# Performance work log

Hardware: AMD Instinct MI355X
Metric: run time of the kernel (lower is better)

Reference implementation:

```python
import jax, jax.numpy as jnp
import numpy as np
import math

B, I, O, D, H = 32, 1152, 10, 16, 10
SUB = 0.8
S = math.ceil(SUB * I)  # 922 subset size


def _safe_l2norm(x, axis, keepdims=False):
    # L2 norm with zero-safe gradient (forward-identical to jnp.linalg.norm)
    s = jnp.sum(x * x, axis=axis, keepdims=keepdims)
    return jnp.where(s == 0, 0.0, jnp.sqrt(jnp.where(s == 0, 1.0, s)))


def setup_inputs() -> dict:
    key = jax.random.key(0)
    k1, k2 = jax.random.split(key)
    u_predict = jax.random.normal(k1, (B, I, O, D), dtype=jnp.float32)
    # emulate torch.rand(...).topk(S, dim=1).indices: top-S distinct indices along input_caps
    noise = jax.random.uniform(k2, (B, I, O, H))
    sample_idx = jnp.argsort(-noise, axis=1)[:, :S].astype(jnp.int64)  # [B,S,O,H]
    return {"u_predict": u_predict, "sample_idx": sample_idx}


def reference(u_predict, sample_idx):
    b, i, o, d = u_predict.shape
    h = sample_idx.shape[-1]
    # scatter 0/1 hypothesis mask r: [B,I,O,H]
    bi = jnp.arange(b)[:, None, None, None]
    oi = jnp.arange(o)[None, None, :, None]
    hi = jnp.arange(h)[None, None, None, :]
    r = jnp.zeros((b, i, o, h), u_predict.dtype).at[bi, sample_idx, oi, hi].set(1.0)

    # Vr = V_exp * r; since r is 0/1, ||Vr||_D = r * ||V||_D
    Vnorm = _safe_l2norm(u_predict, axis=3)            # [B,I,O]
    Vr_norm = Vnorm[..., None] * r                     # [B,I,O,H]
    # Mu = sum_i(Vr_norm * Vr) / sum_i Vr_norm  (Vr_norm*Vr = r*||V||*V since r^2=r)
    num = jnp.einsum('bioh,biod->bodh', Vr_norm, u_predict)   # [B,O,D,H]
    Mu = num / jnp.sum(Vr_norm, axis=1)[:, :, None, :]        # [B,O,D,H]

    # losses = sum_i ||V_exp - Mu||_D  -> [B,O,H]
    diff = u_predict[..., None] - Mu[:, None]          # [B,I,O,D,H]
    losses = jnp.sum(_safe_l2norm(diff, axis=3), axis=1)
    min_idx = jnp.argmin(losses, axis=2)               # [B,O]

    # pick best hypothesis's mask per (batch, output_caps)
    final_r = jnp.take_along_axis(r, min_idx[:, None, :, None], axis=3)  # [B,I,O,1]

    # capsule weighted average
    u = u_predict * final_r
    un = _safe_l2norm(u, axis=3, keepdims=True)        # [B,I,O,1]
    v = jnp.sum(u * un, axis=1) / jnp.sum(un, axis=1)  # [B,O,D]
    return v
```

## Files before the change

### kernel.cpp

```cpp
#include <hip/hip_runtime.h>
#include <math.h>


#define B_    32
#define I_    1152
#define O_    10
#define D_    16
#define H_    10
#define S_    922
#define MASKW 36
#define NT    640

__global__ __launch_bounds__(NT, 1) void ransac_kernel(
    const float* __restrict__ up,
    const int*   __restrict__ sidx,
    float*       __restrict__ out)
{
    __shared__ float    u_t[D_][I_];
    __shared__ float    vn[I_];
    __shared__ unsigned mask[H_][MASKW];
    __shared__ float    Mu[D_][H_];
    __shared__ double   losses[H_];
    __shared__ int      hstar;

    const int bo   = blockIdx.x;
    const int b    = bo / O_;
    const int o    = bo - b * O_;
    const int tid  = threadIdx.x;
    const int lane = tid & 63;
    const int wv   = tid >> 6;

    for (int j = tid; j < H_ * MASKW; j += NT)
        ((unsigned*)mask)[j] = 0u;
    __syncthreads();

    const int* sb = sidx + (size_t)b * (S_ * O_ * H_) + o * H_;
    for (int j = tid; j < S_ * H_; j += NT) {
        int s = j / H_;
        int h = j - s * H_;
        int idx = sb[s * (O_ * H_) + h];
        atomicOr(&mask[h][idx >> 5], 1u << (idx & 31));
    }

    const float* ub = up + (size_t)b * (I_ * O_ * D_) + o * D_;
    for (int i = tid; i < I_; i += NT) {
        const float4* p = (const float4*)(ub + (size_t)i * (O_ * D_));
        float4 q0 = p[0], q1 = p[1], q2 = p[2], q3 = p[3];
        float s = q0.x*q0.x + q0.y*q0.y + q0.z*q0.z + q0.w*q0.w
                + q1.x*q1.x + q1.y*q1.y + q1.z*q1.z + q1.w*q1.w
                + q2.x*q2.x + q2.y*q2.y + q2.z*q2.z + q2.w*q2.w
                + q3.x*q3.x + q3.y*q3.y + q3.z*q3.z + q3.w*q3.w;
        vn[i] = sqrtf(s);
        u_t[ 0][i]=q0.x; u_t[ 1][i]=q0.y; u_t[ 2][i]=q0.z; u_t[ 3][i]=q0.w;
        u_t[ 4][i]=q1.x; u_t[ 5][i]=q1.y; u_t[ 6][i]=q1.z; u_t[ 7][i]=q1.w;
        u_t[ 8][i]=q2.x; u_t[ 9][i]=q2.y; u_t[10][i]=q2.z; u_t[11][i]=q2.w;
        u_t[12][i]=q3.x; u_t[13][i]=q3.y; u_t[14][i]=q3.z; u_t[15][i]=q3.w;
    }
    __syncthreads();

    const int h = wv;
    float num[D_];
    #pragma unroll
    for (int d = 0; d < D_; ++d) num[d] = 0.f;
    float den = 0.f;
    for (int i = lane; i < I_; i += 64) {
        unsigned bit = (mask[h][i >> 5] >> (i & 31)) & 1u;
        float w = bit ? vn[i] : 0.f;
        den += w;
        #pragma unroll
        for (int d = 0; d < D_; ++d) num[d] = fmaf(w, u_t[d][i], num[d]);
    }
    #pragma unroll
    for (int off = 32; off; off >>= 1) {
        den += __shfl_xor(den, off, 64);
        #pragma unroll
        for (int d = 0; d < D_; ++d) num[d] += __shfl_xor(num[d], off, 64);
    }
    if (lane == 0) {
        float rd = 1.f / den;
        #pragma unroll
        for (int d = 0; d < D_; ++d) Mu[d][h] = num[d] * rd;
    }
    __syncthreads();

    float muh[D_];
    #pragma unroll
    for (int d = 0; d < D_; ++d) muh[d] = Mu[d][h];
    double loss = 0.0;
    for (int i = lane; i < I_; i += 64) {
        float ss = 0.f;
        #pragma unroll
        for (int d = 0; d < D_; ++d) {
            float df = u_t[d][i] - muh[d];
            ss = fmaf(df, df, ss);
        }
        loss += sqrt((double)ss);
    }
    #pragma unroll
    for (int off = 32; off; off >>= 1)
        loss += __shfl_xor(loss, off, 64);
    if (lane == 0) losses[h] = loss;
    __syncthreads();

    if (tid == 0) {
        int best = 0; double bl = losses[0];
        #pragma unroll
        for (int hh = 1; hh < H_; ++hh)
            if (losses[hh] < bl) { bl = losses[hh]; best = hh; }
        hstar = best;
    }
    __syncthreads();

    if (tid < D_)
        out[(size_t)bo * D_ + tid] = Mu[tid][hstar];
}

extern "C" void kernel_launch(void* const* d_in, const int* in_sizes, int n_in,
                              void* d_out, int out_size, void* d_ws, size_t ws_size,
                              hipStream_t stream) {
    const float* up   = (const float*)d_in[0];
    const int*   sidx = (const int*)d_in[1];
    float*       out  = (float*)d_out;
    ransac_kernel<<<B_ * O_, NT, 0, stream>>>(up, sidx, out);
}
```

Before: 113.0 us.

## Compute hypothesis means via complement lists and expand loss distances algebraically

```diff
diff --git a/kernel.cpp b/kernel.cpp
--- a/kernel.cpp
+++ b/kernel.cpp
@@ -8,41 +8,82 @@
 #define D_    16
 #define H_    10
 #define S_    922
+#define COMP  230
 #define MASKW 36
-#define NT    640
-
-__global__ __launch_bounds__(NT, 1) void ransac_kernel(
+#define NT    512
+#define NW    8
+
+__device__ __forceinline__ int uoff(int i, int c) {
+    return i * 16 + (((c ^ ((i >> 1) & 3)) & 3) << 2);
+}
+
+template <int CTRL, int ROWM>
+static __device__ __forceinline__ float dpp_f(float v) {
+    return __int_as_float(__builtin_amdgcn_update_dpp(
+        0, __float_as_int(v), CTRL, ROWM, 0xf, true));
+}
+static __device__ __forceinline__ float wave_sum_f32(float v) {
+    v += dpp_f<0x111, 0xf>(v);
+    v += dpp_f<0x112, 0xf>(v);
+    v += dpp_f<0x114, 0xf>(v);
+    v += dpp_f<0x118, 0xf>(v);
+    v += dpp_f<0x142, 0xa>(v);
+    v += dpp_f<0x143, 0xc>(v);
+    return v;
+}
+template <int CTRL, int ROWM>
+static __device__ __forceinline__ double dpp_d(double v) {
+    long long x = __double_as_longlong(v);
+    int lo = (int)(unsigned)(x & 0xffffffffLL);
+    int hi = (int)(x >> 32);
+    lo = __builtin_amdgcn_update_dpp(0, lo, CTRL, ROWM, 0xf, true);
+    hi = __builtin_amdgcn_update_dpp(0, hi, CTRL, ROWM, 0xf, true);
+    return __longlong_as_double((long long)(unsigned)lo | ((long long)hi << 32));
+}
+static __device__ __forceinline__ double wave_sum_f64(double v) {
+    v += dpp_d<0x111, 0xf>(v);
+    v += dpp_d<0x112, 0xf>(v);
+    v += dpp_d<0x114, 0xf>(v);
+    v += dpp_d<0x118, 0xf>(v);
+    v += dpp_d<0x142, 0xa>(v);
+    v += dpp_d<0x143, 0xc>(v);
+    return v;
+}
+
+__global__ __launch_bounds__(NT, 2) void ransac_kernel(
     const float* __restrict__ up,
     const int*   __restrict__ sidx,
     float*       __restrict__ out)
 {
-    __shared__ float    u_t[D_][I_];
-    __shared__ float    vn[I_];
-    __shared__ unsigned mask[H_][MASKW];
-    __shared__ float    Mu[D_][H_];
-    __shared__ double   losses[H_];
-    __shared__ int      hstar;
-
-    const int bo   = blockIdx.x;
-    const int b    = bo / O_;
-    const int o    = bo - b * O_;
+    __shared__ float          u_s[I_ * 16];
+    __shared__ unsigned       mask[H_][MASKW];
+    __shared__ unsigned short clist[H_][COMP];
+    __shared__ int            ccount[H_];
+    __shared__ float          Mu_s[H_][D_];
+    __shared__ float          totred[NW][17];
+    __shared__ float          tot[17];
+    __shared__ double         lpart[H_][NW];
+    __shared__ double         losses[H_];
+    __shared__ int            hstar;
+
+    const int blk = blockIdx.x;
+    const int xcd = blk & 7, g = blk >> 3;
+    const int b   = xcd + 8 * (g / O_);
+    const int o   = g - O_ * (g / O_);
+    const int bo  = b * O_ + o;
+
     const int tid  = threadIdx.x;
     const int lane = tid & 63;
     const int wv   = tid >> 6;
 
-    for (int j = tid; j < H_ * MASKW; j += NT)
-        ((unsigned*)mask)[j] = 0u;
-    __syncthreads();
-
-    const int* sb = sidx + (size_t)b * (S_ * O_ * H_) + o * H_;
-    for (int j = tid; j < S_ * H_; j += NT) {
-        int s = j / H_;
-        int h = j - s * H_;
-        int idx = sb[s * (O_ * H_) + h];
-        atomicOr(&mask[h][idx >> 5], 1u << (idx & 31));
-    }
-
-    const float* ub = up + (size_t)b * (I_ * O_ * D_) + o * D_;
+    for (int j = tid; j < H_ * MASKW; j += NT) ((unsigned*)mask)[j] = 0u;
+    if (tid < H_) ccount[tid] = 0;
+    __syncthreads();
+
+    const float* ub = up + ((size_t)b * I_ * O_ + o) * D_;
+    float acc[D_]; float accd = 0.f;
+    #pragma unroll
+    for (int d = 0; d < D_; ++d) acc[d] = 0.f;
     for (int i = tid; i < I_; i += NT) {
         const float4* p = (const float4*)(ub + (size_t)i * (O_ * D_));
         float4 q0 = p[0], q1 = p[1], q2 = p[2], q3 = p[3];
@@ -50,69 +91,170 @@
                 + q1.x*q1.x + q1.y*q1.y + q1.z*q1.z + q1.w*q1.w
                 + q2.x*q2.x + q2.y*q2.y + q2.z*q2.z + q2.w*q2.w
                 + q3.x*q3.x + q3.y*q3.y + q3.z*q3.z + q3.w*q3.w;
-        vn[i] = sqrtf(s);
-        u_t[ 0][i]=q0.x; u_t[ 1][i]=q0.y; u_t[ 2][i]=q0.z; u_t[ 3][i]=q0.w;
-        u_t[ 4][i]=q1.x; u_t[ 5][i]=q1.y; u_t[ 6][i]=q1.z; u_t[ 7][i]=q1.w;
-        u_t[ 8][i]=q2.x; u_t[ 9][i]=q2.y; u_t[10][i]=q2.z; u_t[11][i]=q2.w;
-        u_t[12][i]=q3.x; u_t[13][i]=q3.y; u_t[14][i]=q3.z; u_t[15][i]=q3.w;
-    }
-    __syncthreads();
-
-    const int h = wv;
-    float num[D_];
-    #pragma unroll
-    for (int d = 0; d < D_; ++d) num[d] = 0.f;
-    float den = 0.f;
-    for (int i = lane; i < I_; i += 64) {
-        unsigned bit = (mask[h][i >> 5] >> (i & 31)) & 1u;
-        float w = bit ? vn[i] : 0.f;
-        den += w;
-        #pragma unroll
-        for (int d = 0; d < D_; ++d) num[d] = fmaf(w, u_t[d][i], num[d]);
-    }
-    #pragma unroll
-    for (int off = 32; off; off >>= 1) {
-        den += __shfl_xor(den, off, 64);
-        #pragma unroll
-        for (int d = 0; d < D_; ++d) num[d] += __shfl_xor(num[d], off, 64);
-    }
-    if (lane == 0) {
-        float rd = 1.f / den;
-        #pragma unroll
-        for (int d = 0; d < D_; ++d) Mu[d][h] = num[d] * rd;
-    }
-    __syncthreads();
-
-    float muh[D_];
-    #pragma unroll
-    for (int d = 0; d < D_; ++d) muh[d] = Mu[d][h];
-    double loss = 0.0;
-    for (int i = lane; i < I_; i += 64) {
-        float ss = 0.f;
-        #pragma unroll
-        for (int d = 0; d < D_; ++d) {
-            float df = u_t[d][i] - muh[d];
-            ss = fmaf(df, df, ss);
-        }
-        loss += sqrt((double)ss);
-    }
-    #pragma unroll
-    for (int off = 32; off; off >>= 1)
-        loss += __shfl_xor(loss, off, 64);
-    if (lane == 0) losses[h] = loss;
-    __syncthreads();
-
+        float vn = sqrtf(s);
+        *(float4*)&u_s[uoff(i,0)] = q0;
+        *(float4*)&u_s[uoff(i,1)] = q1;
+        *(float4*)&u_s[uoff(i,2)] = q2;
+        *(float4*)&u_s[uoff(i,3)] = q3;
+        acc[ 0] = fmaf(vn, q0.x, acc[ 0]); acc[ 1] = fmaf(vn, q0.y, acc[ 1]);
+        acc[ 2] = fmaf(vn, q0.z, acc[ 2]); acc[ 3] = fmaf(vn, q0.w, acc[ 3]);
+        acc[ 4] = fmaf(vn, q1.x, acc[ 4]); acc[ 5] = fmaf(vn, q1.y, acc[ 5]);
+        acc[ 6] = fmaf(vn, q1.z, acc[ 6]); acc[ 7] = fmaf(vn, q1.w, acc[ 7]);
+        acc[ 8] = fmaf(vn, q2.x, acc[ 8]); acc[ 9] = fmaf(vn, q2.y, acc[ 9]);
+        acc[10] = fmaf(vn, q2.z, acc[10]); acc[11] = fmaf(vn, q2.w, acc[11]);
+        acc[12] = fmaf(vn, q3.x, acc[12]); acc[13] = fmaf(vn, q3.y, acc[13]);
+        acc[14] = fmaf(vn, q3.z, acc[14]); acc[15] = fmaf(vn, q3.w, acc[15]);
+        accd += vn;
+    }
+
+    const int* sb = sidx + (size_t)b * (S_ * O_ * H_) + o * H_;
+    for (int j = tid; j < S_ * H_; j += NT) {
+        int s = j / H_;
+        int h = j - s * H_;
+        int idx = sb[s * (O_ * H_) + h];
+        atomicOr(&mask[h][idx >> 5], 1u << (idx & 31));
+    }
+
+    #pragma unroll
+    for (int d = 0; d < D_; ++d) acc[d] = wave_sum_f32(acc[d]);
+    accd = wave_sum_f32(accd);
+    if (lane == 63) {
+        #pragma unroll
+        for (int d = 0; d < D_; ++d) totred[wv][d] = acc[d];
+        totred[wv][16] = accd;
+    }
+    __syncthreads();
+
+    if (tid < 17) {
+        float t = 0.f;
+        #pragma unroll
+        for (int w = 0; w < NW; ++w) t += totred[w][tid];
+        tot[tid] = t;
+    }
+
+    for (int h = wv; h < H_; h += NW) {
+        if (lane < MASKW) {
+            unsigned m = ~mask[h][lane];
+            int cnt = __popc(m);
+            int base = atomicAdd(&ccount[h], cnt);
+            while (m) {
+                int bit = __ffs(m) - 1;
+                m &= m - 1u;
+                clist[h][base++] = (unsigned short)((lane << 5) + bit);
+            }
+        }
+    }
+    __syncthreads();
+
+    for (int h = wv; h < H_; h += NW) {
+        float na[D_]; float nd = 0.f;
+        #pragma unroll
+        for (int d = 0; d < D_; ++d) na[d] = 0.f;
+        for (int k = lane; k < COMP; k += 64) {
+            int i = clist[h][k];
+            float4 q0 = *(const float4*)&u_s[uoff(i,0)];
+            float4 q1 = *(const float4*)&u_s[uoff(i,1)];
+            float4 q2 = *(const float4*)&u_s[uoff(i,2)];
+            float4 q3 = *(const float4*)&u_s[uoff(i,3)];
+            float s = q0.x*q0.x + q0.y*q0.y + q0.z*q0.z + q0.w*q0.w
+                    + q1.x*q1.x + q1.y*q1.y + q1.z*q1.z + q1.w*q1.w
+                    + q2.x*q2.x + q2.y*q2.y + q2.z*q2.z + q2.w*q2.w
+                    + q3.x*q3.x + q3.y*q3.y + q3.z*q3.z + q3.w*q3.w;
+            float vn = sqrtf(s);
+            na[ 0] = fmaf(vn, q0.x, na[ 0]); na[ 1] = fmaf(vn, q0.y, na[ 1]);
+            na[ 2] = fmaf(vn, q0.z, na[ 2]); na[ 3] = fmaf(vn, q0.w, na[ 3]);
+            na[ 4] = fmaf(vn, q1.x, na[ 4]); na[ 5] = fmaf(vn, q1.y, na[ 5]);
+            na[ 6] = fmaf(vn, q1.z, na[ 6]); na[ 7] = fmaf(vn, q1.w, na[ 7]);
+            na[ 8] = fmaf(vn, q2.x, na[ 8]); na[ 9] = fmaf(vn, q2.y, na[ 9]);
+            na[10] = fmaf(vn, q2.z, na[10]); na[11] = fmaf(vn, q2.w, na[11]);
+            na[12] = fmaf(vn, q3.x, na[12]); na[13] = fmaf(vn, q3.y, na[13]);
+            na[14] = fmaf(vn, q3.z, na[14]); na[15] = fmaf(vn, q3.w, na[15]);
+            nd += vn;
+        }
+        #pragma unroll
+        for (int d = 0; d < D_; ++d) na[d] = wave_sum_f32(na[d]);
+        nd = wave_sum_f32(nd);
+        if (lane == 63) {
+            float rd = 1.f / (tot[16] - nd);
+            #pragma unroll
+            for (int d = 0; d < D_; ++d)
+                Mu_s[h][d] = (tot[d] - na[d]) * rd;
+        }
+    }
+    __syncthreads();
+
+    float mu[H_][D_];
+    #pragma unroll
+    for (int h = 0; h < H_; ++h) {
+        float4 m0 = *(const float4*)&Mu_s[h][0];
+        float4 m1 = *(const float4*)&Mu_s[h][4];
+        float4 m2 = *(const float4*)&Mu_s[h][8];
+        float4 m3 = *(const float4*)&Mu_s[h][12];
+        mu[h][ 0]=m0.x; mu[h][ 1]=m0.y; mu[h][ 2]=m0.z; mu[h][ 3]=m0.w;
+        mu[h][ 4]=m1.x; mu[h][ 5]=m1.y; mu[h][ 6]=m1.z; mu[h][ 7]=m1.w;
+        mu[h][ 8]=m2.x; mu[h][ 9]=m2.y; mu[h][10]=m2.z; mu[h][11]=m2.w;
+        mu[h][12]=m3.x; mu[h][13]=m3.y; mu[h][14]=m3.z; mu[h][15]=m3.w;
+    }
+    float musq[H_];
+    #pragma unroll
+    for (int h = 0; h < H_; ++h) {
+        float s = 0.f;
+        #pragma unroll
+        for (int d = 0; d < D_; ++d) s = fmaf(mu[h][d], mu[h][d], s);
+        musq[h] = s;
+    }
+    double lacc[H_];
+    #pragma unroll
+    for (int h = 0; h < H_; ++h) lacc[h] = 0.0;
+
+    auto lossStep = [&](int i) {
+        float4 q0 = *(const float4*)&u_s[uoff(i,0)];
+        float4 q1 = *(const float4*)&u_s[uoff(i,1)];
+        float4 q2 = *(const float4*)&u_s[uoff(i,2)];
+        float4 q3 = *(const float4*)&u_s[uoff(i,3)];
+        float uq[D_] = {q0.x,q0.y,q0.z,q0.w, q1.x,q1.y,q1.z,q1.w,
+                        q2.x,q2.y,q2.z,q2.w, q3.x,q3.y,q3.z,q3.w};
+        float usq = 0.f;
+        #pragma unroll
+        for (int d = 0; d < D_; ++d) usq = fmaf(uq[d], uq[d], usq);
+        #pragma unroll
+        for (int h = 0; h < H_; ++h) {
+            float dot = 0.f;
+            #pragma unroll
+            for (int d = 0; d < D_; ++d) dot = fmaf(uq[d], mu[h][d], dot);
+            float d2 = fmaf(-2.f, dot, usq + musq[h]);
+            lacc[h] += (double)sqrtf(fmaxf(d2, 0.f));
+        }
+    };
+    lossStep(tid);
+    lossStep(tid + NT);
+    if (tid >= 384) lossStep(tid + 640);
+
+    #pragma unroll
+    for (int h = 0; h < H_; ++h) lacc[h] = wave_sum_f64(lacc[h]);
+    if (lane == 63) {
+        #pragma unroll
+        for (int h = 0; h < H_; ++h) lpart[h][wv] = lacc[h];
+    }
+    __syncthreads();
+
+    if (tid < H_) {
+        double t = 0.0;
+        #pragma unroll
+        for (int w = 0; w < NW; ++w) t += lpart[tid][w];
+        losses[tid] = t;
+    }
+    __syncthreads();
     if (tid == 0) {
         int best = 0; double bl = losses[0];
         #pragma unroll
-        for (int hh = 1; hh < H_; ++hh)
-            if (losses[hh] < bl) { bl = losses[hh]; best = hh; }
+        for (int h = 1; h < H_; ++h)
+            if (losses[h] < bl) { bl = losses[h]; best = h; }
         hstar = best;
     }
     __syncthreads();
-
     if (tid < D_)
-        out[(size_t)bo * D_ + tid] = Mu[tid][hstar];
+        out[(size_t)bo * D_ + tid] = Mu_s[hstar][tid];
 }
 
 extern "C" void kernel_launch(void* const* d_in, const int* in_sizes, int n_in,
```

After: 107.0 us. 5.3% less time.

## Keep capsule rows in registers, use per-row hypothesis bitmasks and DPP reductions

Applied to the files above, without the earlier changes.

```diff
diff --git a/kernel.cpp b/kernel.cpp
--- a/kernel.cpp
+++ b/kernel.cpp
@@ -2,36 +2,102 @@
 #include <math.h>
 
 
-#define B_    32
-#define I_    1152
-#define O_    10
-#define D_    16
-#define H_    10
-#define S_    922
-#define MASKW 36
-#define NT    640
-
-__global__ __launch_bounds__(NT, 1) void ransac_kernel(
+#define B_ 32
+#define I_ 1152
+#define O_ 10
+#define H_ 10
+#define S_ 922
+#define D_ 16
+#define NT 512
+
+template <int CTRL, int ROWM>
+static __device__ __forceinline__ float dpp_f(float v) {
+    return __int_as_float(__builtin_amdgcn_update_dpp(
+        0, __float_as_int(v), CTRL, ROWM, 0xf, true));
+}
+static __device__ __forceinline__ float wave_sum_f32(float v) {
+    v += dpp_f<0x111, 0xf>(v);
+    v += dpp_f<0x112, 0xf>(v);
+    v += dpp_f<0x114, 0xf>(v);
+    v += dpp_f<0x118, 0xf>(v);
+    v += dpp_f<0x142, 0xa>(v);
+    v += dpp_f<0x143, 0xc>(v);
+    return v;
+}
+template <int CTRL, int ROWM>
+static __device__ __forceinline__ double dpp_d(double v) {
+    long long x = __double_as_longlong(v);
+    int lo = (int)(unsigned)(x & 0xffffffffLL);
+    int hi = (int)(x >> 32);
+    lo = __builtin_amdgcn_update_dpp(0, lo, CTRL, ROWM, 0xf, true);
+    hi = __builtin_amdgcn_update_dpp(0, hi, CTRL, ROWM, 0xf, true);
+    return __longlong_as_double((long long)(unsigned)lo | ((long long)hi << 32));
+}
+static __device__ __forceinline__ double wave_sum_f64(double v) {
+    v += dpp_d<0x111, 0xf>(v);
+    v += dpp_d<0x112, 0xf>(v);
+    v += dpp_d<0x114, 0xf>(v);
+    v += dpp_d<0x118, 0xf>(v);
+    v += dpp_d<0x142, 0xa>(v);
+    v += dpp_d<0x143, 0xc>(v);
+    return v;
+}
+
+__global__ __launch_bounds__(NT) void ransac_one(
     const float* __restrict__ up,
     const int*   __restrict__ sidx,
     float*       __restrict__ out)
 {
-    __shared__ float    u_t[D_][I_];
-    __shared__ float    vn[I_];
-    __shared__ unsigned mask[H_][MASKW];
-    __shared__ float    Mu[D_][H_];
+    __shared__ unsigned rowmask[I_];
+    __shared__ float    red[8][34];
+    __shared__ float    muL[H_][D_];
+    __shared__ double   lred[H_][8];
     __shared__ double   losses[H_];
     __shared__ int      hstar;
 
-    const int bo   = blockIdx.x;
-    const int b    = bo / O_;
-    const int o    = bo - b * O_;
+    const int g   = blockIdx.x;
+    const int xcd = g & 7, r = g >> 3;
+    const int bhi = r / O_;
+    const int o   = r - bhi * O_;
+    const int b   = bhi * 8 + xcd;
+    const int bo  = b * O_ + o;
+
     const int tid  = threadIdx.x;
     const int lane = tid & 63;
     const int wv   = tid >> 6;
-
-    for (int j = tid; j < H_ * MASKW; j += NT)
-        ((unsigned*)mask)[j] = 0u;
+    const bool has3 = (tid < 128);
+
+    for (int j = tid; j < I_; j += NT) rowmask[j] = 0u;
+
+    const float* ub = up + (((size_t)b * I_) * O_ + o) * D_;
+    float u0[D_], u1[D_], u2[D_];
+    {
+        const float4* p = (const float4*)(ub + (size_t)tid * (O_ * D_));
+        float4 a = p[0], bq = p[1], c = p[2], dq = p[3];
+        u0[0]=a.x; u0[1]=a.y; u0[2]=a.z; u0[3]=a.w;
+        u0[4]=bq.x; u0[5]=bq.y; u0[6]=bq.z; u0[7]=bq.w;
+        u0[8]=c.x; u0[9]=c.y; u0[10]=c.z; u0[11]=c.w;
+        u0[12]=dq.x; u0[13]=dq.y; u0[14]=dq.z; u0[15]=dq.w;
+    }
+    {
+        const float4* p = (const float4*)(ub + (size_t)(tid + 512) * (O_ * D_));
+        float4 a = p[0], bq = p[1], c = p[2], dq = p[3];
+        u1[0]=a.x; u1[1]=a.y; u1[2]=a.z; u1[3]=a.w;
+        u1[4]=bq.x; u1[5]=bq.y; u1[6]=bq.z; u1[7]=bq.w;
+        u1[8]=c.x; u1[9]=c.y; u1[10]=c.z; u1[11]=c.w;
+        u1[12]=dq.x; u1[13]=dq.y; u1[14]=dq.z; u1[15]=dq.w;
+    }
+    if (has3) {
+        const float4* p = (const float4*)(ub + (size_t)(tid + 1024) * (O_ * D_));
+        float4 a = p[0], bq = p[1], c = p[2], dq = p[3];
+        u2[0]=a.x; u2[1]=a.y; u2[2]=a.z; u2[3]=a.w;
+        u2[4]=bq.x; u2[5]=bq.y; u2[6]=bq.z; u2[7]=bq.w;
+        u2[8]=c.x; u2[9]=c.y; u2[10]=c.z; u2[11]=c.w;
+        u2[12]=dq.x; u2[13]=dq.y; u2[14]=dq.z; u2[15]=dq.w;
+    } else {
+        #pragma unroll
+        for (int d = 0; d < D_; ++d) u2[d] = 0.f;
+    }
     __syncthreads();
 
     const int* sb = sidx + (size_t)b * (S_ * O_ * H_) + o * H_;
@@ -39,80 +105,144 @@
         int s = j / H_;
         int h = j - s * H_;
         int idx = sb[s * (O_ * H_) + h];
-        atomicOr(&mask[h][idx >> 5], 1u << (idx & 31));
-    }
-
-    const float* ub = up + (size_t)b * (I_ * O_ * D_) + o * D_;
-    for (int i = tid; i < I_; i += NT) {
-        const float4* p = (const float4*)(ub + (size_t)i * (O_ * D_));
-        float4 q0 = p[0], q1 = p[1], q2 = p[2], q3 = p[3];
-        float s = q0.x*q0.x + q0.y*q0.y + q0.z*q0.z + q0.w*q0.w
-                + q1.x*q1.x + q1.y*q1.y + q1.z*q1.z + q1.w*q1.w
-                + q2.x*q2.x + q2.y*q2.y + q2.z*q2.z + q2.w*q2.w
-                + q3.x*q3.x + q3.y*q3.y + q3.z*q3.z + q3.w*q3.w;
-        vn[i] = sqrtf(s);
-        u_t[ 0][i]=q0.x; u_t[ 1][i]=q0.y; u_t[ 2][i]=q0.z; u_t[ 3][i]=q0.w;
-        u_t[ 4][i]=q1.x; u_t[ 5][i]=q1.y; u_t[ 6][i]=q1.z; u_t[ 7][i]=q1.w;
-        u_t[ 8][i]=q2.x; u_t[ 9][i]=q2.y; u_t[10][i]=q2.z; u_t[11][i]=q2.w;
-        u_t[12][i]=q3.x; u_t[13][i]=q3.y; u_t[14][i]=q3.z; u_t[15][i]=q3.w;
-    }
-    __syncthreads();
-
-    const int h = wv;
-    float num[D_];
-    #pragma unroll
-    for (int d = 0; d < D_; ++d) num[d] = 0.f;
-    float den = 0.f;
-    for (int i = lane; i < I_; i += 64) {
-        unsigned bit = (mask[h][i >> 5] >> (i & 31)) & 1u;
-        float w = bit ? vn[i] : 0.f;
-        den += w;
-        #pragma unroll
-        for (int d = 0; d < D_; ++d) num[d] = fmaf(w, u_t[d][i], num[d]);
-    }
-    #pragma unroll
-    for (int off = 32; off; off >>= 1) {
-        den += __shfl_xor(den, off, 64);
-        #pragma unroll
-        for (int d = 0; d < D_; ++d) num[d] += __shfl_xor(num[d], off, 64);
-    }
-    if (lane == 0) {
-        float rd = 1.f / den;
-        #pragma unroll
-        for (int d = 0; d < D_; ++d) Mu[d][h] = num[d] * rd;
-    }
-    __syncthreads();
-
-    float muh[D_];
-    #pragma unroll
-    for (int d = 0; d < D_; ++d) muh[d] = Mu[d][h];
-    double loss = 0.0;
-    for (int i = lane; i < I_; i += 64) {
-        float ss = 0.f;
+        atomicOr(&rowmask[idx], 1u << h);
+    }
+    __syncthreads();
+
+    const unsigned rm0 = rowmask[tid];
+    const unsigned rm1 = rowmask[tid + 512];
+    const unsigned rm2 = has3 ? rowmask[tid + 1024] : 0u;
+
+    float vn0, vn1, vn2;
+    {
+        float s0 = 0.f, s1 = 0.f, s2 = 0.f;
         #pragma unroll
         for (int d = 0; d < D_; ++d) {
-            float df = u_t[d][i] - muh[d];
-            ss = fmaf(df, df, ss);
-        }
-        loss += sqrt((double)ss);
-    }
-    #pragma unroll
-    for (int off = 32; off; off >>= 1)
-        loss += __shfl_xor(loss, off, 64);
-    if (lane == 0) losses[h] = loss;
-    __syncthreads();
-
+            s0 = fmaf(u0[d], u0[d], s0);
+            s1 = fmaf(u1[d], u1[d], s1);
+            s2 = fmaf(u2[d], u2[d], s2);
+        }
+        vn0 = sqrtf(s0); vn1 = sqrtf(s1); vn2 = sqrtf(s2);
+    }
+
+    #pragma unroll 1
+    for (int p = 0; p < 5; ++p) {
+        const int h0 = 2 * p;
+        float acc[34];
+        #pragma unroll
+        for (int v = 0; v < 34; ++v) acc[v] = 0.f;
+
+        {
+            unsigned m = rm0 >> h0;
+            float w0 = (m & 1u) ? vn0 : 0.f;
+            float w1 = (m & 2u) ? vn0 : 0.f;
+            #pragma unroll
+            for (int d = 0; d < D_; ++d) {
+                acc[d]      = fmaf(w0, u0[d], acc[d]);
+                acc[17 + d] = fmaf(w1, u0[d], acc[17 + d]);
+            }
+            acc[16] += w0; acc[33] += w1;
+        }
+        {
+            unsigned m = rm1 >> h0;
+            float w0 = (m & 1u) ? vn1 : 0.f;
+            float w1 = (m & 2u) ? vn1 : 0.f;
+            #pragma unroll
+            for (int d = 0; d < D_; ++d) {
+                acc[d]      = fmaf(w0, u1[d], acc[d]);
+                acc[17 + d] = fmaf(w1, u1[d], acc[17 + d]);
+            }
+            acc[16] += w0; acc[33] += w1;
+        }
+        if (has3) {
+            unsigned m = rm2 >> h0;
+            float w0 = (m & 1u) ? vn2 : 0.f;
+            float w1 = (m & 2u) ? vn2 : 0.f;
+            #pragma unroll
+            for (int d = 0; d < D_; ++d) {
+                acc[d]      = fmaf(w0, u2[d], acc[d]);
+                acc[17 + d] = fmaf(w1, u2[d], acc[17 + d]);
+            }
+            acc[16] += w0; acc[33] += w1;
+        }
+
+        #pragma unroll
+        for (int v = 0; v < 34; ++v) acc[v] = wave_sum_f32(acc[v]);
+        if (lane == 63) {
+            #pragma unroll
+            for (int v = 0; v < 34; ++v) red[wv][v] = acc[v];
+        }
+        __syncthreads();
+
+        if (tid < 34) {
+            const int p2 = tid / 17, e = tid - 17 * p2;
+            float s = 0.f;
+            #pragma unroll
+            for (int w = 0; w < 8; ++w) s += red[w][tid];
+            if (e < 16) {
+                float den = 0.f;
+                #pragma unroll
+                for (int w = 0; w < 8; ++w) den += red[w][p2 * 17 + 16];
+                muL[h0 + p2][e] = s / den;
+            }
+        }
+        __syncthreads();
+    }
+
+    const float usq0 = vn0 * vn0, usq1 = vn1 * vn1, usq2 = vn2 * vn2;
+    #pragma unroll 1
+    for (int h = 0; h < H_; ++h) {
+        float mh[D_];
+        {
+            float4 a = *(const float4*)&muL[h][0];
+            float4 bq = *(const float4*)&muL[h][4];
+            float4 c = *(const float4*)&muL[h][8];
+            float4 dq = *(const float4*)&muL[h][12];
+            mh[0]=a.x; mh[1]=a.y; mh[2]=a.z; mh[3]=a.w;
+            mh[4]=bq.x; mh[5]=bq.y; mh[6]=bq.z; mh[7]=bq.w;
+            mh[8]=c.x; mh[9]=c.y; mh[10]=c.z; mh[11]=c.w;
+            mh[12]=dq.x; mh[13]=dq.y; mh[14]=dq.z; mh[15]=dq.w;
+        }
+        float musq = 0.f;
+        #pragma unroll
+        for (int d = 0; d < D_; ++d) musq = fmaf(mh[d], mh[d], musq);
+
+        float dot0 = 0.f, dot1 = 0.f, dot2 = 0.f;
+        #pragma unroll
+        for (int d = 0; d < D_; ++d) {
+            dot0 = fmaf(u0[d], mh[d], dot0);
+            dot1 = fmaf(u1[d], mh[d], dot1);
+            dot2 = fmaf(u2[d], mh[d], dot2);
+        }
+        float d20 = fmaf(-2.f, dot0, usq0 + musq);
+        float d21 = fmaf(-2.f, dot1, usq1 + musq);
+        float d22 = fmaf(-2.f, dot2, usq2 + musq);
+        double lacc = (double)sqrtf(fmaxf(d20, 0.f))
+                    + (double)sqrtf(fmaxf(d21, 0.f));
+        if (has3) lacc += (double)sqrtf(fmaxf(d22, 0.f));
+
+        lacc = wave_sum_f64(lacc);
+        if (lane == 63) lred[h][wv] = lacc;
+    }
+    __syncthreads();
+
+    if (tid < H_) {
+        double t = 0.0;
+        #pragma unroll
+        for (int w = 0; w < 8; ++w) t += lred[tid][w];
+        losses[tid] = t;
+    }
+    __syncthreads();
     if (tid == 0) {
         int best = 0; double bl = losses[0];
         #pragma unroll
-        for (int hh = 1; hh < H_; ++hh)
-            if (losses[hh] < bl) { bl = losses[hh]; best = hh; }
+        for (int h = 1; h < H_; ++h)
+            if (losses[h] < bl) { bl = losses[h]; best = h; }
         hstar = best;
     }
     __syncthreads();
-
     if (tid < D_)
-        out[(size_t)bo * D_ + tid] = Mu[tid][hstar];
+        out[(size_t)bo * D_ + tid] = muL[hstar][tid];
 }
 
 extern "C" void kernel_launch(void* const* d_in, const int* in_sizes, int n_in,
@@ -121,5 +251,5 @@
     const float* up   = (const float*)d_in[0];
     const int*   sidx = (const int*)d_in[1];
     float*       out  = (float*)d_out;
-    ransac_kernel<<<B_ * O_, NT, 0, stream>>>(up, sidx, out);
-}
+    ransac_one<<<B_ * O_, NT, 0, stream>>>(up, sidx, out);
+}
```

Result: slower. 115.3 us (+2.0%).
